# Performance work log

Hardware: AMD Instinct MI355X
Metric: run time of the kernel (lower is better)

The kernel has to match this reference:

```python
import jax, jax.numpy as jnp
import numpy as np

NUM_LEVELS = 1024
EMBED_DIM = 256
BOUND_LEVELS = NUM_LEVELS // 2  # int(num_levels / 2)


def setup_inputs() -> dict:
    key = jax.random.key(0)
    kz, kc = jax.random.split(key)
    z = jax.random.normal(kz, (131072, EMBED_DIM), dtype=jnp.float32)
    codebook = 0.1 * jax.random.normal(kc, (NUM_LEVELS, EMBED_DIM), dtype=jnp.float32)
    temperature = jnp.float32(1.0)          # registered buffer, init 1.0
    usage_count = jnp.zeros((NUM_LEVELS,), dtype=jnp.float32)  # buffer, init 0
    return {"z": z, "codebook": codebook, "temperature": temperature, "usage_count": usage_count}


def _entropy_rate(usage_count):
    total = usage_count.sum()
    probs = usage_count / jnp.maximum(total, jnp.float32(1e-10))
    ent = -(probs * jnp.log2(probs + 1e-10)).sum()
    return jnp.where(total > 0, ent, jnp.float32(0.0))


def reference(z, codebook, temperature, usage_count):
    # bounding: bound_levels * tanh(z / T), then round * T
    bounded = BOUND_LEVELS * jnp.tanh(z / temperature)
    q = jnp.round(bounded) * temperature                       # [N, D]
    # cdist + argmin: squared distances give identical argmin (sqrt is monotone)
    d2 = (jnp.sum(q * q, axis=-1, keepdims=True)
          - 2.0 * jnp.einsum('nd,kd->nk', q, codebook)
          + jnp.sum(codebook * codebook, axis=-1))             # [N, K]
    assignments = jnp.argmin(d2, axis=1)                       # [N] int
    # straight-through estimator
    quantized = z + jax.lax.stop_gradient(q - z)
    commitment_loss = jnp.mean((z - jax.lax.stop_gradient(quantized)) ** 2) / temperature
    codebook_loss = jnp.mean((quantized - jax.lax.stop_gradient(z)) ** 2) / temperature
    entropy_loss = -_entropy_rate(usage_count) * 0.1
    total_loss = commitment_loss + codebook_loss + entropy_loss
    return quantized, total_loss
```

## Files before the change

### kernel.cpp

```cpp
#include <hip/hip_runtime.h>
#include <math.h>

constexpr int N_TOK   = 131072;
constexpr int EMB     = 256;
constexpr long long N_ELEMS = (long long)N_TOK * EMB;
constexpr int NUM_LEVELS = 1024;
constexpr float BOUND = 512.0f;

constexpr int BLOCK = 256;
constexpr int GRID  = 4096;
constexpr int V4    = (int)(N_ELEMS / 4);
constexpr int PER_THREAD = V4 / (BLOCK * GRID);

typedef float v4f __attribute__((ext_vector_type(4)));

__device__ __forceinline__ float bounded_fast(float zc) {
    float e = __expf(zc);
    float r = __builtin_amdgcn_rcpf(e + 1.0f);
    return fmaf(-1024.0f, r, 512.0f);
}

__global__ __launch_bounds__(BLOCK) void fsq_main(
    const v4f* __restrict__ z4,
    const float* __restrict__ temp,
    v4f*       __restrict__ out4,
    double*    __restrict__ partials)
{
    const float T  = temp[0];
    const float c  = 2.0f / T;

    float local = 0.0f;
    const int base = blockIdx.x * BLOCK + threadIdx.x;

    #pragma unroll
    for (int i = 0; i < PER_THREAD; ++i) {
        const int idx = base + i * (GRID * BLOCK);
        v4f zv = z4[idx];
        v4f qv;
        qv.x = rintf(bounded_fast(zv.x * c)) * T;
        qv.y = rintf(bounded_fast(zv.y * c)) * T;
        qv.z = rintf(bounded_fast(zv.z * c)) * T;
        qv.w = rintf(bounded_fast(zv.w * c)) * T;
        __builtin_nontemporal_store(qv, &out4[idx]);
        float dx = zv.x - qv.x;
        float dy = zv.y - qv.y;
        float dz = zv.z - qv.z;
        float dw = zv.w - qv.w;
        local += dx * dx + dy * dy + dz * dz + dw * dw;
    }

    #pragma unroll
    for (int off = 32; off > 0; off >>= 1)
        local += __shfl_down(local, off, 64);

    __shared__ double smem[BLOCK / 64];
    if ((threadIdx.x & 63) == 0) smem[threadIdx.x >> 6] = (double)local;
    __syncthreads();
    if (threadIdx.x == 0) {
        double s = 0.0;
        #pragma unroll
        for (int w = 0; w < BLOCK / 64; ++w) s += smem[w];
        partials[blockIdx.x] = s;
    }
}

__global__ __launch_bounds__(256) void fsq_loss(
    const double* __restrict__ partials,
    const float*  __restrict__ usage,
    const float*  __restrict__ temp,
    float*        __restrict__ loss_out)
{
    const int tid = threadIdx.x;

    __shared__ double sd[256];
    __shared__ float  sf[256];

    double s = 0.0;
    for (int i = tid; i < GRID; i += 256) s += partials[i];
    sd[tid] = s;
    __syncthreads();
    for (int off = 128; off > 0; off >>= 1) {
        if (tid < off) sd[tid] += sd[tid + off];
        __syncthreads();
    }
    const double sum_sq = sd[0];
    __syncthreads();

    float ut = 0.0f;
    for (int i = tid; i < NUM_LEVELS; i += 256) ut += usage[i];
    sf[tid] = ut;
    __syncthreads();
    for (int off = 128; off > 0; off >>= 1) {
        if (tid < off) sf[tid] += sf[tid + off];
        __syncthreads();
    }
    const float total = sf[0];
    __syncthreads();

    const float inv_total = 1.0f / fmaxf(total, 1e-10f);
    float e = 0.0f;
    for (int i = tid; i < NUM_LEVELS; i += 256) {
        float p = usage[i] * inv_total;
        e += p * log2f(p + 1e-10f);
    }
    sf[tid] = e;
    __syncthreads();
    for (int off = 128; off > 0; off >>= 1) {
        if (tid < off) sf[tid] += sf[tid + off];
        __syncthreads();
    }

    if (tid == 0) {
        float ent = -sf[0];
        float ent_rate = (total > 0.0f) ? ent : 0.0f;
        float entropy_loss = -ent_rate * 0.1f;
        float T = temp[0];
        double mean = sum_sq / (double)N_ELEMS;
        loss_out[0] = (float)(2.0 * mean / (double)T) + entropy_loss;
    }
}

extern "C" void kernel_launch(void* const* d_in, const int* in_sizes, int n_in,
                              void* d_out, int out_size, void* d_ws, size_t ws_size,
                              hipStream_t stream) {
    const float* z     = (const float*)d_in[0];
    const float* temp  = (const float*)d_in[2];
    const float* usage = (const float*)d_in[3];

    float*  out      = (float*)d_out;
    double* partials = (double*)d_ws;

    fsq_main<<<GRID, BLOCK, 0, stream>>>(
        (const v4f*)z, temp, (v4f*)out, partials);

    fsq_loss<<<1, 256, 0, stream>>>(
        partials, usage, temp, out + N_ELEMS);
}
```

Before: 252.5 us.

## Use one float4 per thread with global double atomic reduction

Launches one thread per float4 (32768 blocks) in place of a fixed 4096-block grid where each thread looped over eight float4s. Per-block partial sums are added straight into one double via atomicAdd after a memset, so the final kernel no longer reduces a partials array. The nontemporal store becomes a normal store. The risks are extra block-launch overhead, 32768 atomics contending on a single address, an added memset launch, and sums that vary slightly from run to run.

Measured after the change: 572.3 us. +126.7%, slower.

```diff
diff --git a/kernel.cpp b/kernel.cpp
--- a/kernel.cpp
+++ b/kernel.cpp
@@ -5,12 +5,10 @@
 constexpr int EMB     = 256;
 constexpr long long N_ELEMS = (long long)N_TOK * EMB;
 constexpr int NUM_LEVELS = 1024;
-constexpr float BOUND = 512.0f;
 
 constexpr int BLOCK = 256;
-constexpr int GRID  = 4096;
 constexpr int V4    = (int)(N_ELEMS / 4);
-constexpr int PER_THREAD = V4 / (BLOCK * GRID);
+constexpr int GRID  = V4 / BLOCK;
 
 typedef float v4f __attribute__((ext_vector_type(4)));
 
@@ -24,67 +22,48 @@
     const v4f* __restrict__ z4,
     const float* __restrict__ temp,
     v4f*       __restrict__ out4,
-    double*    __restrict__ partials)
+    double*    __restrict__ acc)
 {
-    const float T  = temp[0];
-    const float c  = 2.0f / T;
+    const float T = temp[0];
+    const float c = 2.0f / T;
 
-    float local = 0.0f;
-    const int base = blockIdx.x * BLOCK + threadIdx.x;
+    const int idx = blockIdx.x * BLOCK + threadIdx.x;
+    v4f zv = z4[idx];
+    v4f qv;
+    qv.x = rintf(bounded_fast(zv.x * c)) * T;
+    qv.y = rintf(bounded_fast(zv.y * c)) * T;
+    qv.z = rintf(bounded_fast(zv.z * c)) * T;
+    qv.w = rintf(bounded_fast(zv.w * c)) * T;
+    out4[idx] = qv;
 
-    #pragma unroll
-    for (int i = 0; i < PER_THREAD; ++i) {
-        const int idx = base + i * (GRID * BLOCK);
-        v4f zv = z4[idx];
-        v4f qv;
-        qv.x = rintf(bounded_fast(zv.x * c)) * T;
-        qv.y = rintf(bounded_fast(zv.y * c)) * T;
-        qv.z = rintf(bounded_fast(zv.z * c)) * T;
-        qv.w = rintf(bounded_fast(zv.w * c)) * T;
-        __builtin_nontemporal_store(qv, &out4[idx]);
-        float dx = zv.x - qv.x;
-        float dy = zv.y - qv.y;
-        float dz = zv.z - qv.z;
-        float dw = zv.w - qv.w;
-        local += dx * dx + dy * dy + dz * dz + dw * dw;
-    }
+    float dx = zv.x - qv.x;
+    float dy = zv.y - qv.y;
+    float dz = zv.z - qv.z;
+    float dw = zv.w - qv.w;
+    float local = dx * dx + dy * dy + dz * dz + dw * dw;
 
     #pragma unroll
     for (int off = 32; off > 0; off >>= 1)
         local += __shfl_down(local, off, 64);
 
-    __shared__ double smem[BLOCK / 64];
-    if ((threadIdx.x & 63) == 0) smem[threadIdx.x >> 6] = (double)local;
+    __shared__ float smem[BLOCK / 64];
+    if ((threadIdx.x & 63) == 0) smem[threadIdx.x >> 6] = local;
     __syncthreads();
     if (threadIdx.x == 0) {
-        double s = 0.0;
-        #pragma unroll
-        for (int w = 0; w < BLOCK / 64; ++w) s += smem[w];
-        partials[blockIdx.x] = s;
+        double s = (double)smem[0] + (double)smem[1]
+                 + (double)smem[2] + (double)smem[3];
+        atomicAdd(acc, s);
     }
 }
 
 __global__ __launch_bounds__(256) void fsq_loss(
-    const double* __restrict__ partials,
+    const double* __restrict__ acc,
     const float*  __restrict__ usage,
     const float*  __restrict__ temp,
     float*        __restrict__ loss_out)
 {
     const int tid = threadIdx.x;
-
-    __shared__ double sd[256];
-    __shared__ float  sf[256];
-
-    double s = 0.0;
-    for (int i = tid; i < GRID; i += 256) s += partials[i];
-    sd[tid] = s;
-    __syncthreads();
-    for (int off = 128; off > 0; off >>= 1) {
-        if (tid < off) sd[tid] += sd[tid + off];
-        __syncthreads();
-    }
-    const double sum_sq = sd[0];
-    __syncthreads();
+    __shared__ float sf[256];
 
     float ut = 0.0f;
     for (int i = tid; i < NUM_LEVELS; i += 256) ut += usage[i];
@@ -115,7 +94,7 @@
         float ent_rate = (total > 0.0f) ? ent : 0.0f;
         float entropy_loss = -ent_rate * 0.1f;
         float T = temp[0];
-        double mean = sum_sq / (double)N_ELEMS;
+        double mean = acc[0] / (double)N_ELEMS;
         loss_out[0] = (float)(2.0 * mean / (double)T) + entropy_loss;
     }
 }
@@ -127,12 +106,14 @@
     const float* temp  = (const float*)d_in[2];
     const float* usage = (const float*)d_in[3];
 
-    float*  out      = (float*)d_out;
-    double* partials = (double*)d_ws;
+    float*  out = (float*)d_out;
+    double* acc = (double*)d_ws;
+
+    hipMemsetAsync(acc, 0, sizeof(double), stream);
 
     fsq_main<<<GRID, BLOCK, 0, stream>>>(
-        (const v4f*)z, temp, (v4f*)out, partials);
+        (const v4f*)z, temp, (v4f*)out, acc);
 
     fsq_loss<<<1, 256, 0, stream>>>(
-        partials, usage, temp, out + N_ELEMS);
+        acc, usage, temp, out + N_ELEMS);
 }
```
